# Kernel tuning notes

Hardware: AMD Instinct MI355X
Metric: run time of the kernel (lower is better)

## Reference

```python
import jax, jax.numpy as jnp
import numpy as np

B, S, WIDTH, H = 4, 1024, 1024, 16
DH = WIDTH // H
NEG = -1000000000.0


def setup_inputs() -> dict:
    key = jax.random.key(0)
    ks = jax.random.split(key, 11)
    sc = 0.02
    return {
        "inp": jax.random.normal(ks[0], (B, S, WIDTH), dtype=jnp.float32),
        "mask": jax.random.randint(ks[1], (B, 1, S, S), 0, 2, dtype=jnp.int32),
        "wq": jax.random.normal(ks[2], (WIDTH, WIDTH), dtype=jnp.float32) * sc,
        "bq": jax.random.normal(ks[3], (WIDTH,), dtype=jnp.float32) * sc,
        "wk": jax.random.normal(ks[4], (WIDTH, WIDTH), dtype=jnp.float32) * sc,
        "bk": jax.random.normal(ks[5], (WIDTH,), dtype=jnp.float32) * sc,
        "wv": jax.random.normal(ks[6], (WIDTH, WIDTH), dtype=jnp.float32) * sc,
        "bv": jax.random.normal(ks[7], (WIDTH,), dtype=jnp.float32) * sc,
        "wo": jax.random.normal(ks[8], (WIDTH, WIDTH), dtype=jnp.float32) * sc,
        "bo": jax.random.normal(ks[9], (WIDTH,), dtype=jnp.float32) * sc,
    }


def reference(inp, mask, wq, bq, wk, bk, wv, bv, wo, bo):
    # torch Linear: y = x @ W.T + b
    q = inp @ wq.T + bq  # [B,S,WIDTH]
    k = inp @ wk.T + bk
    v = inp @ wv.T + bv
    # split heads -> [B,H,S,DH]
    q = q.reshape(B, S, H, DH).transpose(0, 2, 1, 3)
    k = k.reshape(B, S, H, DH).transpose(0, 2, 1, 3)
    v = v.reshape(B, S, H, DH).transpose(0, 2, 1, 3)
    scale = 1.0 / jnp.sqrt(jnp.float32(DH))
    qk = jnp.einsum("bhqd,bhkd->bhqk", q, k) * scale  # [B,H,S,S]
    qk = jnp.where(mask == 0, jnp.float32(NEG), qk)
    # NOTE: faithful to source, softmax over dim=1 (the HEAD axis), not keys
    attn = jax.nn.softmax(qk, axis=1)
    x = jnp.einsum("bhqk,bhkd->bhqd", attn, v)  # [B,H,S,DH]
    x = x.transpose(0, 2, 1, 3).reshape(B, S, WIDTH)
    return x @ wo.T + bo
```

## Files before the change

kernel.cpp:

```cpp
#include <hip/hip_runtime.h>


typedef float f32x4 __attribute__((ext_vector_type(4)));
typedef __bf16 bf16x8 __attribute__((ext_vector_type(8)));

__device__ __forceinline__ unsigned short f2bf(float f){
  unsigned int u = __builtin_bit_cast(unsigned int, f);
  u = (u + 0x7FFFu + ((u >> 16) & 1u)) >> 16;
  return (unsigned short)u;
}

__global__ __launch_bounds__(256) void cvt_kernel(const float* __restrict__ s,
                                                  unsigned short* __restrict__ d, int n4){
  int i = blockIdx.x * 256 + threadIdx.x;
  if (i < n4){
    float4 v = ((const float4*)s)[i];
    ushort4 o;
    o.x = f2bf(v.x); o.y = f2bf(v.y); o.z = f2bf(v.z); o.w = f2bf(v.w);
    ((ushort4*)d)[i] = o;
  }
}

#define BM 128
#define BN 128
#define BK 32
#define LDP 40

template<int MODE>
__global__ __launch_bounds__(256) void gemm_bt(
    const unsigned short* __restrict__ A, const unsigned short* __restrict__ Wt,
    int M, int N, int K,
    float* __restrict__ outp,
    unsigned short* __restrict__ qws, unsigned short* __restrict__ kws,
    unsigned short* __restrict__ vws,
    const float* __restrict__ bias0, const float* __restrict__ bias1,
    const float* __restrict__ bias2)
{
  __shared__ unsigned short Asm_[BM*LDP];
  __shared__ unsigned short Wsm_[BN*LDP];
  const int tid = threadIdx.x;
  const int lane = tid & 63;
  const int wid = tid >> 6;
  const int wr = wid >> 1, wc = wid & 1;
  const int m0 = blockIdx.x * BM, n0 = blockIdx.y * BN;
  const int lq = lane & 15, lg = lane >> 4;
  const int r0 = tid >> 2;
  const int cb = (tid & 3) * 8;
  f32x4 acc[4][4] = {};

  for (int k0 = 0; k0 < K; k0 += BK){
    uint4 av0 = *(const uint4*)(A  + (size_t)(m0 + r0)*K      + k0 + cb);
    uint4 wv0 = *(const uint4*)(Wt + (size_t)(n0 + r0)*K      + k0 + cb);
    uint4 av1 = *(const uint4*)(A  + (size_t)(m0 + r0 + 64)*K + k0 + cb);
    uint4 wv1 = *(const uint4*)(Wt + (size_t)(n0 + r0 + 64)*K + k0 + cb);
    *(uint4*)(&Asm_[ r0      *LDP + cb]) = av0;
    *(uint4*)(&Wsm_[ r0      *LDP + cb]) = wv0;
    *(uint4*)(&Asm_[(r0 + 64)*LDP + cb]) = av1;
    *(uint4*)(&Wsm_[(r0 + 64)*LDP + cb]) = wv1;
    __syncthreads();
    bf16x8 af[4], wf[4];
    #pragma unroll
    for (int i = 0; i < 4; ++i){
      af[i] = *(const bf16x8*)(&Asm_[(wr*64 + i*16 + lq)*LDP + lg*8]);
      wf[i] = *(const bf16x8*)(&Wsm_[(wc*64 + i*16 + lq)*LDP + lg*8]);
    }
    #pragma unroll
    for (int i = 0; i < 4; ++i)
      #pragma unroll
      for (int j = 0; j < 4; ++j)
        acc[i][j] = __builtin_amdgcn_mfma_f32_16x16x32_bf16(af[i], wf[j], acc[i][j], 0, 0, 0);
    __syncthreads();
  }

  if (MODE == 0){
    #pragma unroll
    for (int j = 0; j < 4; ++j){
      int ncol = n0 + wc*64 + j*16 + lq;
      float bv = bias0[ncol];
      #pragma unroll
      for (int i = 0; i < 4; ++i){
        int mrow = m0 + wr*64 + i*16 + lg*4;
        #pragma unroll
        for (int r = 0; r < 4; ++r)
          outp[(size_t)(mrow + r)*N + ncol] = acc[i][j][r] + bv;
      }
    }
  } else {
    const int sel = n0 >> 10;
    const float* bp = (sel == 0) ? bias0 : ((sel == 1) ? bias1 : bias2);
    #pragma unroll
    for (int j = 0; j < 4; ++j){
      int n  = n0 + wc*64 + j*16 + lq;
      int n1 = n & 1023;
      int h = n1 >> 6, d = n1 & 63;
      float bv = bp[n1];
      #pragma unroll
      for (int i = 0; i < 4; ++i){
        int mbase = m0 + wr*64 + i*16 + lg*4;
        #pragma unroll
        for (int r = 0; r < 4; ++r){
          int m = mbase + r;
          int b = m >> 10, s = m & 1023;
          unsigned short o = f2bf(acc[i][j][r] + bv);
          if (sel == 0)      qws[(size_t)((((b<<4) + h)<<10) + s)*64 + d] = o;
          else if (sel == 1) kws[(size_t)((((b<<4) + h)<<10) + s)*64 + d] = o;
          else               vws[(size_t)((((b<<4) + h)<<6) + d)*1024 + s] = o;
        }
      }
    }
  }
}

__global__ __launch_bounds__(512) void qksm_kernel(
    const unsigned short* __restrict__ qws, const unsigned short* __restrict__ kws,
    const int* __restrict__ mask, unsigned short* __restrict__ pws, int qbase)
{
  __shared__ unsigned short Qs[16*16*64];
  const int tid = threadIdx.x;
  const int lane = tid & 63, w = tid >> 6;
  const int kt = blockIdx.x, qt = blockIdx.y, b = blockIdx.z;
  const int q0 = qbase + (qt << 4);
  const int lq = lane & 15, lg = lane >> 4;
  const int aswz = (lq & 7) << 4;

  for (int c = tid; c < 2048; c += 512){
    int e = c << 3;
    int h = e >> 10, q = (e >> 6) & 15, d0 = e & 63;
    uint4 v = *(const uint4*)(qws + (size_t)((((b<<4) + h)<<10) + q0 + q)*64 + d0);
    int byteoff = (((h<<10) + (q<<6) + d0) << 1) ^ ((q & 7) << 4);
    *(uint4*)((char*)Qs + byteoff) = v;
  }
  __syncthreads();

  const float kscale = 0.125f * 1.44269504f;
  for (int it = 0; it < 2; ++it){
    const int kb = (kt << 8) + (it << 7) + (w << 4);
    f32x4 sc[16];
    #pragma unroll
    for (int h = 0; h < 16; ++h){
      int abase = (h << 11) + (lq << 7) + (lg << 4);
      bf16x8 a0 = *(const bf16x8*)((const char*)Qs + ((abase     ) ^ aswz));
      bf16x8 a1 = *(const bf16x8*)((const char*)Qs + ((abase + 64) ^ aswz));
      const unsigned short* kp = kws + (size_t)((((b<<4) + h)<<10) + kb + lq)*64 + (lg<<3);
      bf16x8 kf0 = *(const bf16x8*)(kp);
      bf16x8 kf1 = *(const bf16x8*)(kp + 32);
      f32x4 s = {};
      s = __builtin_amdgcn_mfma_f32_16x16x32_bf16(a0, kf0, s, 0, 0, 0);
      s = __builtin_amdgcn_mfma_f32_16x16x32_bf16(a1, kf1, s, 0, 0, 0);
      sc[h] = s;
    }
    const int* mp = mask + (size_t)((b<<10) + q0 + (lg<<2))*1024 + kb + lq;
    #pragma unroll
    for (int r = 0; r < 4; ++r){
      const int mv = mp[r << 10];
      float mx = sc[0][r];
      #pragma unroll
      for (int h = 1; h < 16; ++h) mx = fmaxf(mx, sc[h][r]);
      float e[16]; float sum = 0.f;
      #pragma unroll
      for (int h = 0; h < 16; ++h){
        e[h] = __builtin_amdgcn_exp2f((sc[h][r] - mx) * kscale);
        sum += e[h];
      }
      const float rs = __builtin_amdgcn_rcpf(sum);
      const int qloc = (qt << 4) + (lg << 2) + r;
      const size_t pbase = ((size_t)(((b<<4) << 9)) + ((size_t)qloc)) << 10;
      #pragma unroll
      for (int h = 0; h < 16; ++h){
        float pv = mv ? (e[h] * rs) : 0.0625f;
        pws[pbase + ((size_t)h << 19) + kb + lq] = f2bf(pv);
      }
    }
  }
}

__global__ __launch_bounds__(256) void pv_kernel(
    const unsigned short* __restrict__ pws, const unsigned short* __restrict__ vws,
    unsigned short* __restrict__ xbf, int qbase)
{
  __shared__ unsigned short Pt[64*LDP];
  __shared__ unsigned short Vt[64*LDP];
  const int tid = threadIdx.x;
  const int lane = tid & 63;
  const int wid = tid >> 6;
  const int wr = wid >> 1, wc = wid & 1;
  const int qt = blockIdx.x, bh = blockIdx.y;
  const int b = bh >> 4, h = bh & 15;
  const int lq = lane & 15, lg = lane >> 4;
  const int r0 = tid >> 2;
  const int cb = (tid & 3) * 8;
  const unsigned short* Ap = pws + ((size_t)bh << 19) + ((size_t)(qt << 6) << 10);
  const unsigned short* Bp = vws + ((size_t)bh << 16);
  f32x4 acc[2][2] = {};

  for (int k0 = 0; k0 < 1024; k0 += BK){
    uint4 av = *(const uint4*)(Ap + (size_t)r0*1024 + k0 + cb);
    uint4 bv = *(const uint4*)(Bp + (size_t)r0*1024 + k0 + cb);
    *(uint4*)(&Pt[r0*LDP + cb]) = av;
    *(uint4*)(&Vt[r0*LDP + cb]) = bv;
    __syncthreads();
    bf16x8 af[2], wf[2];
    #pragma unroll
    for (int i = 0; i < 2; ++i){
      af[i] = *(const bf16x8*)(&Pt[(wr*32 + i*16 + lq)*LDP + lg*8]);
      wf[i] = *(const bf16x8*)(&Vt[(wc*32 + i*16 + lq)*LDP + lg*8]);
    }
    #pragma unroll
    for (int i = 0; i < 2; ++i)
      #pragma unroll
      for (int j = 0; j < 2; ++j)
        acc[i][j] = __builtin_amdgcn_mfma_f32_16x16x32_bf16(af[i], wf[j], acc[i][j], 0, 0, 0);
    __syncthreads();
  }

  #pragma unroll
  for (int j = 0; j < 2; ++j){
    int d = wc*32 + j*16 + lq;
    #pragma unroll
    for (int i = 0; i < 2; ++i){
      int qrow = qbase + (qt << 6) + wr*32 + i*16 + (lg << 2);
      #pragma unroll
      for (int r = 0; r < 4; ++r)
        xbf[(size_t)((b << 10) + qrow + r)*1024 + (h << 6) + d] = f2bf(acc[i][j][r]);
    }
  }
}

extern "C" void kernel_launch(void* const* d_in, const int* in_sizes, int n_in,
                              void* d_out, int out_size, void* d_ws, size_t ws_size,
                              hipStream_t stream) {
  const float* inp = (const float*)d_in[0];
  const int*  mask = (const int*)d_in[1];
  const float* wq = (const float*)d_in[2];
  const float* bq = (const float*)d_in[3];
  const float* wk = (const float*)d_in[4];
  const float* bk = (const float*)d_in[5];
  const float* wv = (const float*)d_in[6];
  const float* bv = (const float*)d_in[7];
  const float* wo = (const float*)d_in[8];
  const float* bo = (const float*)d_in[9];
  float* out = (float*)d_out;

  char* ws = (char*)d_ws;
  unsigned short* inp_bf = (unsigned short*)(ws);
  unsigned short* wqkv   = (unsigned short*)(ws + (8u  << 20));
  unsigned short* wo_bf  = (unsigned short*)(ws + (14u << 20));
  unsigned short* qws    = (unsigned short*)(ws + (16u << 20));
  unsigned short* kws    = (unsigned short*)(ws + (24u << 20));
  unsigned short* vws    = (unsigned short*)(ws + (32u << 20));
  unsigned short* xbf    = (unsigned short*)(ws + (40u << 20));
  unsigned short* pws    = (unsigned short*)(ws + (48u << 20));

  cvt_kernel<<<4096, 256, 0, stream>>>(inp, inp_bf, 1048576);
  cvt_kernel<<<1024, 256, 0, stream>>>(wq, wqkv,               262144);
  cvt_kernel<<<1024, 256, 0, stream>>>(wk, wqkv + (1u << 20),  262144);
  cvt_kernel<<<1024, 256, 0, stream>>>(wv, wqkv + (2u << 20),  262144);
  cvt_kernel<<<1024, 256, 0, stream>>>(wo, wo_bf, 262144);

  gemm_bt<1><<<dim3(32, 24), 256, 0, stream>>>(inp_bf, wqkv, 4096, 3072, 1024,
                                               nullptr, qws, kws, vws, bq, bk, bv);

  for (int half = 0; half < 2; ++half){
    qksm_kernel<<<dim3(4, 32, 4), 512, 0, stream>>>(qws, kws, mask, pws, half * 512);
    pv_kernel<<<dim3(8, 64), 256, 0, stream>>>(pws, vws, xbf, half * 512);
  }

  gemm_bt<0><<<dim3(32, 8), 256, 0, stream>>>(xbf, wo_bf, 4096, 1024, 1024,
                                              out, nullptr, nullptr, nullptr, bo, nullptr, nullptr);
}
```

Before: 364.3 us.

## Use direct global-to-LDS loads in GEMMs, tile P layout, fuse weight converts

Both GEMMs and the PV kernel now stage tiles into shared memory with global_load_lds 16-byte transfers instead of register round-trips, using unpadded 64-byte rows. The P buffer is rewritten in a key-tiled layout (256-key chunks per 128-query block) so the PV kernel can load 128-row by 32-col tiles contiguously, and PV now computes 128 queries per block with all 64 head dims per wave. The four weight conversions are merged into one launch, and qksm gets a min-occupancy launch bound. Unpadded LDS rows may introduce bank conflicts on the fragment reads.

```diff
diff --git a/kernel.cpp b/kernel.cpp
--- a/kernel.cpp
+++ b/kernel.cpp
@@ -8,6 +8,12 @@
   unsigned int u = __builtin_bit_cast(unsigned int, f);
   u = (u + 0x7FFFu + ((u >> 16) & 1u)) >> 16;
   return (unsigned short)u;
+}
+
+__device__ __forceinline__ void gl16(const unsigned short* g, unsigned short* l){
+  __builtin_amdgcn_global_load_lds(
+      (const __attribute__((address_space(1))) void*)g,
+      (__attribute__((address_space(3))) void*)l, 16, 0, 0);
 }
 
 __global__ __launch_bounds__(256) void cvt_kernel(const float* __restrict__ s,
@@ -21,10 +27,20 @@
   }
 }
 
-#define BM 128
-#define BN 128
-#define BK 32
-#define LDP 40
+__global__ __launch_bounds__(256) void cvt4_kernel(
+    const float* __restrict__ s0, const float* __restrict__ s1,
+    const float* __restrict__ s2, const float* __restrict__ s3,
+    unsigned short* __restrict__ d0, unsigned short* __restrict__ d1,
+    unsigned short* __restrict__ d2, unsigned short* __restrict__ d3){
+  int i = blockIdx.x * 256 + threadIdx.x;
+  int seg = i >> 18, j = i & 262143;
+  const float* s = (seg == 0) ? s0 : (seg == 1) ? s1 : (seg == 2) ? s2 : s3;
+  unsigned short* d = (seg == 0) ? d0 : (seg == 1) ? d1 : (seg == 2) ? d2 : d3;
+  float4 v = ((const float4*)s)[j];
+  ushort4 o;
+  o.x = f2bf(v.x); o.y = f2bf(v.y); o.z = f2bf(v.z); o.w = f2bf(v.w);
+  ((ushort4*)d)[j] = o;
+}
 
 template<int MODE>
 __global__ __launch_bounds__(256) void gemm_bt(
@@ -36,33 +52,33 @@
     const float* __restrict__ bias0, const float* __restrict__ bias1,
     const float* __restrict__ bias2)
 {
-  __shared__ unsigned short Asm_[BM*LDP];
-  __shared__ unsigned short Wsm_[BN*LDP];
+  __shared__ unsigned short As_[128*32];
+  __shared__ unsigned short Bs_[128*32];
   const int tid = threadIdx.x;
   const int lane = tid & 63;
   const int wid = tid >> 6;
   const int wr = wid >> 1, wc = wid & 1;
-  const int m0 = blockIdx.x * BM, n0 = blockIdx.y * BN;
+  const int m0 = blockIdx.x * 128, n0 = blockIdx.y * 128;
   const int lq = lane & 15, lg = lane >> 4;
-  const int r0 = tid >> 2;
-  const int cb = (tid & 3) * 8;
+  const int srow = (wid << 5) + (lane >> 2);
+  const int scol = (lane & 3) << 3;
+  const unsigned short* Ag = A  + (size_t)(m0 + srow)*K + scol;
+  const unsigned short* Bg = Wt + (size_t)(n0 + srow)*K + scol;
+  char* a_l0 = (char*)As_ + (wid << 11);
+  char* b_l0 = (char*)Bs_ + (wid << 11);
   f32x4 acc[4][4] = {};
 
-  for (int k0 = 0; k0 < K; k0 += BK){
-    uint4 av0 = *(const uint4*)(A  + (size_t)(m0 + r0)*K      + k0 + cb);
-    uint4 wv0 = *(const uint4*)(Wt + (size_t)(n0 + r0)*K      + k0 + cb);
-    uint4 av1 = *(const uint4*)(A  + (size_t)(m0 + r0 + 64)*K + k0 + cb);
-    uint4 wv1 = *(const uint4*)(Wt + (size_t)(n0 + r0 + 64)*K + k0 + cb);
-    *(uint4*)(&Asm_[ r0      *LDP + cb]) = av0;
-    *(uint4*)(&Wsm_[ r0      *LDP + cb]) = wv0;
-    *(uint4*)(&Asm_[(r0 + 64)*LDP + cb]) = av1;
-    *(uint4*)(&Wsm_[(r0 + 64)*LDP + cb]) = wv1;
+  for (int k0 = 0; k0 < K; k0 += 32){
+    gl16(Ag + k0,                 (unsigned short*)a_l0);
+    gl16(Ag + (size_t)16*K + k0,  (unsigned short*)(a_l0 + 1024));
+    gl16(Bg + k0,                 (unsigned short*)b_l0);
+    gl16(Bg + (size_t)16*K + k0,  (unsigned short*)(b_l0 + 1024));
     __syncthreads();
     bf16x8 af[4], wf[4];
     #pragma unroll
     for (int i = 0; i < 4; ++i){
-      af[i] = *(const bf16x8*)(&Asm_[(wr*64 + i*16 + lq)*LDP + lg*8]);
-      wf[i] = *(const bf16x8*)(&Wsm_[(wc*64 + i*16 + lq)*LDP + lg*8]);
+      af[i] = *(const bf16x8*)((char*)As_ + ((((wr<<6)+(i<<4)+lq)) << 6) + (lg << 4));
+      wf[i] = *(const bf16x8*)((char*)Bs_ + ((((wc<<6)+(i<<4)+lq)) << 6) + (lg << 4));
     }
     #pragma unroll
     for (int i = 0; i < 4; ++i)
@@ -111,7 +127,7 @@
   }
 }
 
-__global__ __launch_bounds__(512) void qksm_kernel(
+__global__ __launch_bounds__(512, 4) void qksm_kernel(
     const unsigned short* __restrict__ qws, const unsigned short* __restrict__ kws,
     const int* __restrict__ mask, unsigned short* __restrict__ pws, int qbase)
 {
@@ -135,6 +151,7 @@
   const float kscale = 0.125f * 1.44269504f;
   for (int it = 0; it < 2; ++it){
     const int kb = (kt << 8) + (it << 7) + (w << 4);
+    const int klocal = (it << 7) + (w << 4) + lq;
     f32x4 sc[16];
     #pragma unroll
     for (int h = 0; h < 16; ++h){
@@ -164,11 +181,11 @@
       }
       const float rs = __builtin_amdgcn_rcpf(sum);
       const int qloc = (qt << 4) + (lg << 2) + r;
-      const size_t pbase = ((size_t)(((b<<4) << 9)) + ((size_t)qloc)) << 10;
+      unsigned short* pp = pws + (b << 23) + (kt << 17) + (qloc << 8) + klocal;
       #pragma unroll
       for (int h = 0; h < 16; ++h){
         float pv = mv ? (e[h] * rs) : 0.0625f;
-        pws[pbase + ((size_t)h << 19) + kb + lq] = f2bf(pv);
+        pp[h << 19] = f2bf(pv);
       }
     }
   }
@@ -178,50 +195,54 @@
     const unsigned short* __restrict__ pws, const unsigned short* __restrict__ vws,
     unsigned short* __restrict__ xbf, int qbase)
 {
-  __shared__ unsigned short Pt[64*LDP];
-  __shared__ unsigned short Vt[64*LDP];
+  __shared__ unsigned short Ps_[128*32];
+  __shared__ unsigned short Vs_[64*32];
   const int tid = threadIdx.x;
   const int lane = tid & 63;
   const int wid = tid >> 6;
-  const int wr = wid >> 1, wc = wid & 1;
   const int qt = blockIdx.x, bh = blockIdx.y;
   const int b = bh >> 4, h = bh & 15;
   const int lq = lane & 15, lg = lane >> 4;
-  const int r0 = tid >> 2;
-  const int cb = (tid & 3) * 8;
-  const unsigned short* Ap = pws + ((size_t)bh << 19) + ((size_t)(qt << 6) << 10);
-  const unsigned short* Bp = vws + ((size_t)bh << 16);
-  f32x4 acc[2][2] = {};
-
-  for (int k0 = 0; k0 < 1024; k0 += BK){
-    uint4 av = *(const uint4*)(Ap + (size_t)r0*1024 + k0 + cb);
-    uint4 bv = *(const uint4*)(Bp + (size_t)r0*1024 + k0 + cb);
-    *(uint4*)(&Pt[r0*LDP + cb]) = av;
-    *(uint4*)(&Vt[r0*LDP + cb]) = bv;
-    __syncthreads();
-    bf16x8 af[2], wf[2];
+  const int arow = (wid << 5) + (lane >> 2);
+  const int scol = (lane & 3) << 3;
+  const unsigned short* Ag = pws + ((size_t)bh << 19) + (((qt << 7) + arow) << 8) + scol;
+  const int brow = (wid << 4) + (lane >> 2);
+  const unsigned short* Bg = vws + ((size_t)bh << 16) + brow*1024 + scol;
+  char* a_l0 = (char*)Ps_ + (wid << 11);
+  char* b_l0 = (char*)Vs_ + (wid << 10);
+  f32x4 acc[2][4] = {};
+
+  for (int k0 = 0; k0 < 1024; k0 += 32){
+    const int koff = ((k0 >> 8) << 17) + (k0 & 255);
+    gl16(Ag + koff,              (unsigned short*)a_l0);
+    gl16(Ag + koff + (16 << 8),  (unsigned short*)(a_l0 + 1024));
+    gl16(Bg + k0,                (unsigned short*)b_l0);
+    __syncthreads();
+    bf16x8 af[2], wf[4];
+    #pragma unroll
+    for (int i = 0; i < 2; ++i)
+      af[i] = *(const bf16x8*)((char*)Ps_ + ((((wid<<5)+(i<<4)+lq)) << 6) + (lg << 4));
+    #pragma unroll
+    for (int j = 0; j < 4; ++j)
+      wf[j] = *(const bf16x8*)((char*)Vs_ + ((((j<<4)+lq)) << 6) + (lg << 4));
+    #pragma unroll
+    for (int i = 0; i < 2; ++i)
+      #pragma unroll
+      for (int j = 0; j < 4; ++j)
+        acc[i][j] = __builtin_amdgcn_mfma_f32_16x16x32_bf16(af[i], wf[j], acc[i][j], 0, 0, 0);
+    __syncthreads();
+  }
+
+  #pragma unroll
+  for (int j = 0; j < 4; ++j){
+    int d = (j << 4) + lq;
     #pragma unroll
     for (int i = 0; i < 2; ++i){
-      af[i] = *(const bf16x8*)(&Pt[(wr*32 + i*16 + lq)*LDP + lg*8]);
-      wf[i] = *(const bf16x8*)(&Vt[(wc*32 + i*16 + lq)*LDP + lg*8]);
-    }
-    #pragma unroll
-    for (int i = 0; i < 2; ++i)
-      #pragma unroll
-      for (int j = 0; j < 2; ++j)
-        acc[i][j] = __builtin_amdgcn_mfma_f32_16x16x32_bf16(af[i], wf[j], acc[i][j], 0, 0, 0);
-    __syncthreads();
-  }
-
-  #pragma unroll
-  for (int j = 0; j < 2; ++j){
-    int d = wc*32 + j*16 + lq;
-    #pragma unroll
-    for (int i = 0; i < 2; ++i){
-      int qrow = qbase + (qt << 6) + wr*32 + i*16 + (lg << 2);
-      #pragma unroll
-      for (int r = 0; r < 4; ++r)
-        xbf[(size_t)((b << 10) + qrow + r)*1024 + (h << 6) + d] = f2bf(acc[i][j][r]);
+      #pragma unroll
+      for (int r = 0; r < 4; ++r){
+        int qrow = qbase + (qt << 7) + (wid << 5) + (i << 4) + (lg << 2) + r;
+        xbf[(size_t)((b << 10) + qrow)*1024 + (h << 6) + d] = f2bf(acc[i][j][r]);
+      }
     }
   }
 }
@@ -252,17 +273,15 @@
   unsigned short* pws    = (unsigned short*)(ws + (48u << 20));
 
   cvt_kernel<<<4096, 256, 0, stream>>>(inp, inp_bf, 1048576);
-  cvt_kernel<<<1024, 256, 0, stream>>>(wq, wqkv,               262144);
-  cvt_kernel<<<1024, 256, 0, stream>>>(wk, wqkv + (1u << 20),  262144);
-  cvt_kernel<<<1024, 256, 0, stream>>>(wv, wqkv + (2u << 20),  262144);
-  cvt_kernel<<<1024, 256, 0, stream>>>(wo, wo_bf, 262144);
+  cvt4_kernel<<<4096, 256, 0, stream>>>(wq, wk, wv, wo,
+                                        wqkv, wqkv + (1u << 20), wqkv + (2u << 20), wo_bf);
 
   gemm_bt<1><<<dim3(32, 24), 256, 0, stream>>>(inp_bf, wqkv, 4096, 3072, 1024,
                                                nullptr, qws, kws, vws, bq, bk, bv);
 
   for (int half = 0; half < 2; ++half){
     qksm_kernel<<<dim3(4, 32, 4), 512, 0, stream>>>(qws, kws, mask, pws, half * 512);
-    pv_kernel<<<dim3(8, 64), 256, 0, stream>>>(pws, vws, xbf, half * 512);
+    pv_kernel<<<dim3(4, 64), 256, 0, stream>>>(pws, vws, xbf, half * 512);
   }
 
   gemm_bt<0><<<dim3(32, 8), 256, 0, stream>>>(xbf, wo_bf, 4096, 1024, 1024,
```

Measured after the change: 381.6 us. +4.7%, slower.
